# Kernel tuning notes

Hardware: AMD Instinct MI355X
Metric: run time of the kernel (lower is better)

Reference implementation:

```python
import jax, jax.numpy as jnp
import numpy as np

KERNEL_SIZE = 3
FILTERS = 512


def setup_inputs() -> dict:
    key = jax.random.key(0)
    k1, k2 = jax.random.split(key)
    B, T, D, K, F = 8, 2048, 512, KERNEL_SIZE, FILTERS
    x = jax.random.normal(k1, (B, T, D), dtype=jnp.float32)
    kernels = jax.random.normal(k2, (B, T, K, F), dtype=jnp.float32)
    return {"x": x, "kernels": kernels}


def reference(x, kernels):
    # x: [B, T, D], kernels: [B, T, K, F] -> out: [B, T, F]
    B, T, D = x.shape
    K = kernels.shape[2]
    pad = K // 2
    xp = jnp.pad(x, ((0, 0), (pad, pad), (0, 0)))  # [B, T+2*pad, D]
    # Sliding windows along T: patches[b, t, k, d] = xp[b, t + k, d]
    patches = jnp.stack([xp[:, k:k + T, :] for k in range(K)], axis=2)  # [B, T, K, D]
    # Faithful to tf.einsum('btkd,btkf->btf'): sums over BOTH k and d.
    out = jnp.einsum('btkd,btkf->btf', patches, kernels)
    return out
```

## Files before the change

### kernel.cpp

```cpp
#include <hip/hip_runtime.h>
#include <hip/hip_bf16.h>


#define B_ 8
#define T_ 2048
#define D_ 512
#define F_ 512

__global__ __launch_bounds__(256) void rowsum_kernel(
    const float* __restrict__ x, float* __restrict__ S) {
    const int row  = blockIdx.x * 4 + (threadIdx.x >> 6);
    const int lane = threadIdx.x & 63;
    const float4* xr = (const float4*)(x + (size_t)row * D_);
    float4 a = xr[lane];
    float4 b = xr[lane + 64];
    float s = (a.x + a.y) + (a.z + a.w) + (b.x + b.y) + (b.z + b.w);
    #pragma unroll
    for (int off = 32; off > 0; off >>= 1)
        s += __shfl_down(s, off, 64);
    if (lane == 0) S[row] = s;
}

__global__ __launch_bounds__(128) void conv_kernel(
    const float* __restrict__ kern, const float* __restrict__ S,
    float* __restrict__ out) {
    const int bt = blockIdx.x;
    const int t  = bt & (T_ - 1);

    const float s0 = (t > 0)      ? S[bt - 1] : 0.0f;
    const float s1 = S[bt];
    const float s2 = (t < T_ - 1) ? S[bt + 1] : 0.0f;

    const float4* kr = (const float4*)(kern + (size_t)bt * 3 * F_);
    const int i = threadIdx.x;
    float4 k0 = kr[i];
    float4 k1 = kr[i + F_ / 4];
    float4 k2 = kr[i + 2 * (F_ / 4)];

    float4 o;
    o.x = s0 * k0.x + s1 * k1.x + s2 * k2.x;
    o.y = s0 * k0.y + s1 * k1.y + s2 * k2.y;
    o.z = s0 * k0.z + s1 * k1.z + s2 * k2.z;
    o.w = s0 * k0.w + s1 * k1.w + s2 * k2.w;

    ((float4*)(out + (size_t)bt * F_))[i] = o;
}

extern "C" void kernel_launch(void* const* d_in, const int* in_sizes, int n_in,
                              void* d_out, int out_size, void* d_ws, size_t ws_size,
                              hipStream_t stream) {
    const float* x    = (const float*)d_in[0];
    const float* kern = (const float*)d_in[1];
    float* out = (float*)d_out;
    float* S   = (float*)d_ws;

    const int rows = B_ * T_;
    rowsum_kernel<<<rows / 4, 256, 0, stream>>>(x, S);
    conv_kernel<<<rows, 128, 0, stream>>>(kern, S, out);
}
```

Measured before the change: 179.2 us.

## Fuse row-sum and conv into one kernel over time chunks with shared-memory sums

Merges the x row-sum kernel and the per-timestep conv kernel into one launch. Each block handles a 16-timestep chunk: it computes 18 row sums (including halo rows) into shared memory, synchronises, then applies the 3-tap kernels for each timestep. This removes the second launch and the global round trip for the row sums. In exchange, halo rows are recomputed (18/16 reads of x), and the block stalls at the barrier before it starts streaming the kernel tensor.

```diff
diff --git a/kernel.cpp b/kernel.cpp
--- a/kernel.cpp
+++ b/kernel.cpp
@@ -1,49 +1,59 @@
 #include <hip/hip_runtime.h>
-#include <hip/hip_bf16.h>
 
 
 #define B_ 8
 #define T_ 2048
 #define D_ 512
 #define F_ 512
+#define TCHUNK 16
+#define CHUNKS_PER_B (T_ / TCHUNK)
 
-__global__ __launch_bounds__(256) void rowsum_kernel(
-    const float* __restrict__ x, float* __restrict__ S) {
-    const int row  = blockIdx.x * 4 + (threadIdx.x >> 6);
+__global__ __launch_bounds__(256) void fused_conv(
+    const float* __restrict__ x, const float* __restrict__ kern,
+    float* __restrict__ out) {
+    __shared__ float Ssh[TCHUNK + 2];
+
+    const int chunk = blockIdx.x;
+    const int b  = chunk / CHUNKS_PER_B;
+    const int t0 = (chunk - b * CHUNKS_PER_B) * TCHUNK;
+    const int wave = threadIdx.x >> 6;
     const int lane = threadIdx.x & 63;
-    const float4* xr = (const float4*)(x + (size_t)row * D_);
-    float4 a = xr[lane];
-    float4 b = xr[lane + 64];
-    float s = (a.x + a.y) + (a.z + a.w) + (b.x + b.y) + (b.z + b.w);
+
+    for (int r = wave; r < TCHUNK + 2; r += 4) {
+        const int t = t0 - 1 + r;
+        float s = 0.0f;
+        if (t >= 0 && t < T_) {
+            const float4* xr = (const float4*)(x + ((size_t)b * T_ + t) * D_);
+            float4 a = xr[lane];
+            float4 c = xr[lane + 64];
+            s = (a.x + a.y) + (a.z + a.w) + (c.x + c.y) + (c.z + c.w);
+            #pragma unroll
+            for (int off = 32; off > 0; off >>= 1)
+                s += __shfl_down(s, off, 64);
+        }
+        if (lane == 0) Ssh[r] = s;
+    }
+    __syncthreads();
+
+    const int fi   = threadIdx.x & 127;
+    const int rsub = threadIdx.x >> 7;
     #pragma unroll
-    for (int off = 32; off > 0; off >>= 1)
-        s += __shfl_down(s, off, 64);
-    if (lane == 0) S[row] = s;
-}
-
-__global__ __launch_bounds__(128) void conv_kernel(
-    const float* __restrict__ kern, const float* __restrict__ S,
-    float* __restrict__ out) {
-    const int bt = blockIdx.x;
-    const int t  = bt & (T_ - 1);
-
-    const float s0 = (t > 0)      ? S[bt - 1] : 0.0f;
-    const float s1 = S[bt];
-    const float s2 = (t < T_ - 1) ? S[bt + 1] : 0.0f;
-
-    const float4* kr = (const float4*)(kern + (size_t)bt * 3 * F_);
-    const int i = threadIdx.x;
-    float4 k0 = kr[i];
-    float4 k1 = kr[i + F_ / 4];
-    float4 k2 = kr[i + 2 * (F_ / 4)];
-
-    float4 o;
-    o.x = s0 * k0.x + s1 * k1.x + s2 * k2.x;
-    o.y = s0 * k0.y + s1 * k1.y + s2 * k2.y;
-    o.z = s0 * k0.z + s1 * k1.z + s2 * k2.z;
-    o.w = s0 * k0.w + s1 * k1.w + s2 * k2.w;
-
-    ((float4*)(out + (size_t)bt * F_))[i] = o;
+    for (int r = rsub; r < TCHUNK; r += 2) {
+        const size_t bt = (size_t)b * T_ + t0 + r;
+        const float4* kr = (const float4*)(kern + bt * (size_t)(3 * F_));
+        const float s0 = Ssh[r];
+        const float s1 = Ssh[r + 1];
+        const float s2 = Ssh[r + 2];
+        float4 k0 = kr[fi];
+        float4 k1 = kr[fi + (F_ / 4)];
+        float4 k2 = kr[fi + 2 * (F_ / 4)];
+        float4 o;
+        o.x = s0 * k0.x + s1 * k1.x + s2 * k2.x;
+        o.y = s0 * k0.y + s1 * k1.y + s2 * k2.y;
+        o.z = s0 * k0.z + s1 * k1.z + s2 * k2.z;
+        o.w = s0 * k0.w + s1 * k1.w + s2 * k2.w;
+        ((float4*)(out + bt * F_))[fi] = o;
+    }
 }
 
 extern "C" void kernel_launch(void* const* d_in, const int* in_sizes, int n_in,
@@ -52,9 +62,7 @@
     const float* x    = (const float*)d_in[0];
     const float* kern = (const float*)d_in[1];
     float* out = (float*)d_out;
-    float* S   = (float*)d_ws;
+    (void)d_ws; (void)ws_size;
 
-    const int rows = B_ * T_;
-    rowsum_kernel<<<rows / 4, 256, 0, stream>>>(x, S);
-    conv_kernel<<<rows, 128, 0, stream>>>(kern, S, out);
+    fused_conv<<<(B_ * T_) / TCHUNK, 256, 0, stream>>>(x, kern, out);
 }
```

After: 180.7 us. No clear change (+0.9%).
